# Kernel tuning notes

Measured on AMD Instinct MI355X. Metric: run time of the kernel, lower is better.

The kernel has to match this reference:

```python
import jax, jax.numpy as jnp
import numpy as np

N, D, M_COLS, K = 4096, 512, 4096, 2048

def setup_inputs() -> dict:
    key = jax.random.key(0)
    k1, k2, k3 = jax.random.split(key, 3)
    return {
        "in_activations": jax.random.normal(k1, (N, D), dtype=jnp.float32),
        "M": jax.random.normal(k2, (D, M_COLS), dtype=jnp.float32),
        "centroids": jax.random.normal(k3, (K, D), dtype=jnp.float32),
    }

def reference(in_activations, M, centroids):
    # dist[k, m] = || X @ (M[:, m] - c_k) ||_2  over the n sampled activations.
    # Expand || a - b ||^2 = ||a||^2 - 2 a.b + ||b||^2 with a = X@M[:,m], b = X@c_k
    # to avoid materializing the [K, n, m] broadcast tensor of the original.
    XM = in_activations @ M                 # [n, m]
    XC = in_activations @ centroids.T      # [n, K]
    sq = (jnp.sum(XM * XM, axis=0)[None, :]          # [1, m]
          - 2.0 * (XC.T @ XM)                        # [K, m]
          + jnp.sum(XC * XC, axis=0)[:, None])       # [K, 1]
    return jnp.sqrt(jnp.maximum(sq, 0.0))            # [K, m]
```

## Files before the change

kernel.cpp:

```cpp
#include <hip/hip_runtime.h>
#include <stdint.h>

#define NR    4096
#define D_DIM 512
#define MC    4096
#define KC    2048

typedef unsigned short u16;
typedef __attribute__((ext_vector_type(8))) short bf16x8;
typedef __attribute__((ext_vector_type(4))) float f32x4;

__device__ __forceinline__ u16 f2bf(float f) {
  union { float f; uint32_t u; } v; v.f = f;
  return (u16)((v.u + 0x7FFFu + ((v.u >> 16) & 1u)) >> 16);
}
__device__ __forceinline__ float bf2f(u16 h) {
  union { uint32_t u; float f; } v; v.u = (uint32_t)h << 16; return v.f;
}
__device__ __forceinline__ void gload16(const void* g, void* lds) {
  __builtin_amdgcn_global_load_lds((const __attribute__((address_space(1))) void*)g,
                                   (__attribute__((address_space(3))) void*)lds,
                                   16, 0, 0);
}

template <int EPI, int STEPS>
__device__ __forceinline__ void gemm_tile(
    const u16* __restrict__ Ag, const u16* __restrict__ Bg,
    float* __restrict__ Cf, u16* __restrict__ Cbf,
    const u16* __restrict__ DotH, const float* __restrict__ DotF,
    float* __restrict__ vatom, const float* __restrict__ tv, const float* __restrict__ sv,
    int m0, int n0, int Ndim, int Kdim, int kBeg,
    u16* As0, u16* As1, u16* Bs0, u16* Bs1, int tid)
{
  const int rowt = tid >> 3;
  const int cswz = ((tid & 7) ^ ((tid >> 3) & 7)) << 3;
  const int wave = tid >> 6, lane = tid & 63;
  const int wr = (wave >> 1) << 6, wc = (wave & 1) << 6;
  const int fr = lane & 15;
  const int sw = fr & 7;
  const int hq = lane >> 4;
  const int wb = wave << 10;

  f32x4 acc[4][4] = {};
  const u16* agB = Ag + (size_t)(m0 + rowt) * Kdim + cswz;
  const u16* bgB = Bg + (size_t)(n0 + rowt) * Kdim + cswz;

  #define STAGE(k0, Asb, Bsb)                                          \
    _Pragma("unroll")                                                  \
    for (int c = 0; c < 4; ++c) {                                      \
      gload16(agB + (k0) + (size_t)(c * 32) * Kdim, (char*)(Asb) + c * 4096 + wb); \
      gload16(bgB + (k0) + (size_t)(c * 32) * Kdim, (char*)(Bsb) + c * 4096 + wb); \
    }

  STAGE(kBeg, As0, Bs0)

  #pragma unroll
  for (int t = 0; t < STEPS; ++t) {
    u16* Ac = (t & 1) ? As1 : As0;
    u16* Bc = (t & 1) ? Bs1 : Bs0;
    if (t + 1 < STEPS) {
      u16* An = (t & 1) ? As0 : As1;
      u16* Bn = (t & 1) ? Bs0 : Bs1;
      STAGE(kBeg + (t + 1) * 64, An, Bn)
      asm volatile("s_waitcnt vmcnt(8)\n\ts_barrier" ::: "memory");
    } else {
      asm volatile("s_waitcnt vmcnt(0)\n\ts_barrier" ::: "memory");
    }
    __builtin_amdgcn_sched_barrier(0);
    #pragma unroll
    for (int kk = 0; kk < 64; kk += 32) {
      const int so = ((((kk >> 3) + hq) ^ sw) << 3);
      bf16x8 a[4], b[4];
      #pragma unroll
      for (int i = 0; i < 4; ++i) a[i] = *(const bf16x8*)&Ac[(wr + i * 16 + fr) * 64 + so];
      #pragma unroll
      for (int j = 0; j < 4; ++j) b[j] = *(const bf16x8*)&Bc[(wc + j * 16 + fr) * 64 + so];
      #pragma unroll
      for (int i = 0; i < 4; ++i)
        #pragma unroll
        for (int j = 0; j < 4; ++j)
          acc[i][j] = __builtin_amdgcn_mfma_f32_16x16x32_bf16(a[i], b[j], acc[i][j], 0, 0, 0);
    }
    if (t + 1 < STEPS)
      asm volatile("s_barrier" ::: "memory");
  }
  #undef STAGE

  const int q = lane >> 4;
  #pragma unroll
  for (int i = 0; i < 4; ++i) {
    #pragma unroll
    for (int r = 0; r < 4; ++r) {
      const int grow = m0 + wr + i * 16 + q * 4 + r;
      float p = 0.f;
      #pragma unroll
      for (int j = 0; j < 4; ++j) {
        const int gcol = n0 + wc + j * 16 + fr;
        const float v = acc[i][j][r];
        const size_t idx = (size_t)grow * Ndim + gcol;
        if (EPI == 0) Cf[idx] = v;
        if (EPI == 2) { float sq = tv[gcol] - 2.f * v + sv[grow]; Cf[idx] = sqrtf(fmaxf(sq, 0.f)); }
        if (EPI == 3) { Cbf[idx] = f2bf(v); p += v * bf2f(DotH[idx]); }
        if (EPI == 4) { p += v * DotF[idx]; }
      }
      if (EPI == 3 || EPI == 4) {
        #pragma unroll
        for (int off = 1; off < 16; off <<= 1) p += __shfl_xor(p, off);
        if (fr == 0) atomicAdd(&vatom[grow], p);
      }
    }
  }
}

__device__ __forceinline__ void transpose_tile(
    const float* __restrict__ in, u16* __restrict__ out, int R, int C,
    int rt, int ct, int tid, float* tile )
{
  const int tx = tid & 31, ty = tid >> 5;
  #pragma unroll
  for (int i = 0; i < 32; i += 8)
    tile[(size_t)(ty + i) * 33 + tx] = in[(size_t)(rt + ty + i) * C + ct + tx];
  __syncthreads();
  #pragma unroll
  for (int i = 0; i < 32; i += 8)
    out[(size_t)(ct + ty + i) * R + rt + tx] = f2bf(tile[(size_t)tx * 33 + ty + i]);
  __syncthreads();
}

__global__ __launch_bounds__(256)
void xprep(const float* __restrict__ X, u16* __restrict__ XT_bf,
           float* __restrict__ tvec)
{
  __shared__ float tile[32 * 33];
  const int b = blockIdx.x, tid = threadIdx.x;
  int zi = b * 256 + tid;
  if (zi < 4096 + 2048) tvec[zi] = 0.f;
  #pragma unroll 1
  for (int j = 0; j < 4; ++j) {
    int T = b * 4 + j;
    transpose_tile(X, XT_bf, NR, D_DIM, (T >> 4) * 32, (T & 15) * 32, tid, tile);
  }
}

__global__ __launch_bounds__(256)
void gmc(const u16* __restrict__ XT_bf, float* __restrict__ Gpart,
         const float* __restrict__ Mm, const float* __restrict__ Cc,
         u16* __restrict__ M_bfT, u16* __restrict__ C_bf)
{
  __shared__ __align__(16) u16 As[2][8192];
  __shared__ __align__(16) u16 Bs[2][8192];
  const int b = blockIdx.x, tid = threadIdx.x;
  if (b < 256) {
    const int t = b & 15, z = b >> 4;
    const int n0 = (t & 3) * 128, m0 = (t >> 2) * 128;
    gemm_tile<0, 4>(XT_bf, XT_bf, Gpart + (size_t)z * 512 * 512, nullptr, nullptr,
                    nullptr, nullptr, nullptr, nullptr, m0, n0, 512, NR, z * 256,
                    As[0], As[1], Bs[0], Bs[1], tid);
  } else if (b < 768) {
    float* ttile = (float*)As;
    #pragma unroll 1
    for (int j = 0; j < 4; ++j) {
      int T = (b - 256) * 4 + j;
      transpose_tile(Mm, M_bfT, D_DIM, MC, (T >> 7) * 32, (T & 127) * 32, tid, ttile);
    }
  } else {
    const int bb = b - 768;
    const float4* C4 = (const float4*)Cc;
    #pragma unroll 1
    for (int i = bb * 256 + tid; i < (KC * D_DIM) / 4; i += 128 * 256) {
      float4 v = C4[i];
      ushort4 r; r.x = f2bf(v.x); r.y = f2bf(v.y); r.z = f2bf(v.z); r.w = f2bf(v.w);
      *(ushort4*)&C_bf[(size_t)i * 4] = r;
    }
  }
}

__global__ __launch_bounds__(256)
void reduce_g(const float* __restrict__ Gpart, u16* __restrict__ G_bf)
{
  const float4* P4 = (const float4*)Gpart;
  int i = blockIdx.x * 256 + threadIdx.x;
  float4 s = {0.f, 0.f, 0.f, 0.f};
  #pragma unroll
  for (int z = 0; z < 16; ++z) {
    float4 v = P4[(size_t)z * (512 * 512 / 4) + i];
    s.x += v.x; s.y += v.y; s.z += v.z; s.w += v.w;
  }
  ushort4 r; r.x = f2bf(s.x); r.y = f2bf(s.y); r.z = f2bf(s.z); r.w = f2bf(s.w);
  *(ushort4*)&G_bf[(size_t)i * 4] = r;
}

__global__ __launch_bounds__(256)
void mid(const u16* __restrict__ M_bfT, const u16* __restrict__ C_bf,
         const u16* __restrict__ G_bf, const float* __restrict__ Cc,
         u16* __restrict__ A_bfT, float* __restrict__ tvec)
{
  __shared__ __align__(16) u16 As[2][8192];
  __shared__ __align__(16) u16 Bs[2][8192];
  const int b = blockIdx.x, tid = threadIdx.x;
  if (b < 128) {
    const int n0 = (b & 3) * 128, m0 = (b >> 2) * 128;
    gemm_tile<3, 8>(M_bfT, G_bf, nullptr, A_bfT, M_bfT, nullptr, tvec, nullptr, nullptr,
                    m0, n0, 512, 512, 0, As[0], As[1], Bs[0], Bs[1], tid);
  } else {
    const int u = b - 128;
    const int n0 = (u & 3) * 128, m0 = (u >> 2) * 128;
    gemm_tile<4, 8>(C_bf, G_bf, nullptr, nullptr, nullptr, Cc, tvec + 4096, nullptr,
                    nullptr, m0, n0, 512, 512, 0, As[0], As[1], Bs[0], Bs[1], tid);
  }
}

__global__ __launch_bounds__(256)
void final_gemm(const u16* __restrict__ C_bf, const u16* __restrict__ A_bfT,
                const float* __restrict__ tvec, float* __restrict__ out)
{
  __shared__ __align__(16) u16 As[2][8192];
  __shared__ __align__(16) u16 Bs[2][8192];
  const int n0 = blockIdx.x * 128, m0 = blockIdx.y * 128;
  gemm_tile<2, 8>(C_bf, A_bfT, out, nullptr, nullptr, nullptr, nullptr, tvec,
                  tvec + 4096, m0, n0, MC, 512, 0,
                  As[0], As[1], Bs[0], Bs[1], threadIdx.x);
}

extern "C" void kernel_launch(void* const* d_in, const int* in_sizes, int n_in,
                              void* d_out, int out_size, void* d_ws, size_t ws_size,
                              hipStream_t stream) {
  const float* X  = (const float*)d_in[0];
  const float* Mm = (const float*)d_in[1];
  const float* Cc = (const float*)d_in[2];
  float* out = (float*)d_out;

  char* ws = (char*)d_ws;
  const size_t MB = 1u << 20;
  u16*   XT_bf = (u16*)(ws);
  u16*   C_bf  = (u16*)(ws + 4 * MB);
  u16*   M_bfT = (u16*)(ws + 6 * MB);
  u16*   A_bfT = (u16*)(ws + 10 * MB);
  u16*   G_bf  = (u16*)(ws + 14 * MB);
  float* tvec  = (float*)(ws + 14 * MB + 512 * 1024);
  float* Gpart = (float*)(ws + 15 * MB);

  xprep<<<512, 256, 0, stream>>>(X, XT_bf, tvec);
  gmc<<<896, 256, 0, stream>>>(XT_bf, Gpart, Mm, Cc, M_bfT, C_bf);
  reduce_g<<<256, 256, 0, stream>>>(Gpart, G_bf);
  mid<<<192, 256, 0, stream>>>(M_bfT, C_bf, G_bf, Cc, A_bfT, tvec);
  final_gemm<<<dim3(32, 16), 256, 0, stream>>>(C_bf, A_bfT, tvec, out);
}
```

Before: 120.0 us.

## Replace split-K partial buffers and reduce kernel with atomic accumulation into fp32 Gram

The Gram-matrix split-K GEMM now uses 8 K-slices of 512 instead of 16 of 256, and accumulates directly into a zeroed fp32 buffer with atomicAdd instead of writing partials for a separate reduce kernel. The reduce_g launch is removed. The mid kernel gains a variant that loads the fp32 Gram matrix and converts it to bf16 in registers before storing to LDS. This drops one kernel launch and the partial-buffer traffic, at the cost of atomic contention, nondeterministic summation order, and an extra conversion step in mid's B-load path.

```diff
diff --git a/kernel.cpp b/kernel.cpp
--- a/kernel.cpp
+++ b/kernel.cpp
@@ -17,6 +17,9 @@
 __device__ __forceinline__ float bf2f(u16 h) {
   union { uint32_t u; float f; } v; v.u = (uint32_t)h << 16; return v.f;
 }
+__device__ __forceinline__ uint32_t pk2(float a, float b) {
+  return (uint32_t)f2bf(a) | ((uint32_t)f2bf(b) << 16);
+}
 __device__ __forceinline__ void gload16(const void* g, void* lds) {
   __builtin_amdgcn_global_load_lds((const __attribute__((address_space(1))) void*)g,
                                    (__attribute__((address_space(3))) void*)lds,
@@ -26,9 +29,8 @@
 template <int EPI, int STEPS>
 __device__ __forceinline__ void gemm_tile(
     const u16* __restrict__ Ag, const u16* __restrict__ Bg,
-    float* __restrict__ Cf, u16* __restrict__ Cbf,
-    const u16* __restrict__ DotH, const float* __restrict__ DotF,
-    float* __restrict__ vatom, const float* __restrict__ tv, const float* __restrict__ sv,
+    float* __restrict__ Cf,
+    const float* __restrict__ tv, const float* __restrict__ sv,
     int m0, int n0, int Ndim, int Kdim, int kBeg,
     u16* As0, u16* As1, u16* Bs0, u16* Bs1, int tid)
 {
@@ -92,22 +94,120 @@
     #pragma unroll
     for (int r = 0; r < 4; ++r) {
       const int grow = m0 + wr + i * 16 + q * 4 + r;
-      float p = 0.f;
       #pragma unroll
       for (int j = 0; j < 4; ++j) {
         const int gcol = n0 + wc + j * 16 + fr;
         const float v = acc[i][j][r];
         const size_t idx = (size_t)grow * Ndim + gcol;
-        if (EPI == 0) Cf[idx] = v;
+        if (EPI == 1) atomicAdd(&Cf[idx], v);
         if (EPI == 2) { float sq = tv[gcol] - 2.f * v + sv[grow]; Cf[idx] = sqrtf(fmaxf(sq, 0.f)); }
+      }
+    }
+  }
+}
+
+template <int EPI>
+__device__ __forceinline__ void gemm_f32B(
+    const u16* __restrict__ Ag, const float* __restrict__ Gf,
+    u16* __restrict__ Cbf, const u16* __restrict__ DotH,
+    const float* __restrict__ DotF, float* __restrict__ vatom,
+    int m0, int n0,
+    u16* As0, u16* As1, u16* Bs0, u16* Bs1, int tid)
+{
+  const int rowt = tid >> 3;
+  const int cswz = ((tid & 7) ^ ((tid >> 3) & 7)) << 3;
+  const int wave = tid >> 6, lane = tid & 63;
+  const int wr = (wave >> 1) << 6, wc = (wave & 1) << 6;
+  const int fr = lane & 15;
+  const int sw = fr & 7;
+  const int hq = lane >> 4;
+  const int wb = wave << 10;
+  const int bslot = tid & 7;
+  const int bswz = (bslot ^ (rowt & 7)) << 3;
+
+  f32x4 acc[4][4] = {};
+  const u16* agB = Ag + (size_t)(m0 + rowt) * 512 + cswz;
+  const float* gfB = Gf + (size_t)(n0 + rowt) * 512 + bslot * 8;
+
+  float4 breg[4][2];
+
+  #define STAGE_A(k0, Asb)                                             \
+    _Pragma("unroll")                                                  \
+    for (int c = 0; c < 4; ++c)                                        \
+      gload16(agB + (k0) + (size_t)(c * 32) * 512, (char*)(Asb) + c * 4096 + wb);
+
+  #define BLOAD(k0)                                                    \
+    _Pragma("unroll")                                                  \
+    for (int c = 0; c < 4; ++c) {                                      \
+      const float4* p = (const float4*)(gfB + (k0) + (size_t)(c * 32) * 512); \
+      breg[c][0] = p[0]; breg[c][1] = p[1];                            \
+    }
+
+  #define BSTORE(Bsb)                                                  \
+    _Pragma("unroll")                                                  \
+    for (int c = 0; c < 4; ++c) {                                      \
+      uint4 w;                                                         \
+      w.x = pk2(breg[c][0].x, breg[c][0].y);                           \
+      w.y = pk2(breg[c][0].z, breg[c][0].w);                           \
+      w.z = pk2(breg[c][1].x, breg[c][1].y);                           \
+      w.w = pk2(breg[c][1].z, breg[c][1].w);                           \
+      *(uint4*)&(Bsb)[(c * 32 + rowt) * 64 + bswz] = w;                \
+    }
+
+  BLOAD(0)
+  STAGE_A(0, As0)
+  BSTORE(Bs0)
+  __syncthreads();
+
+  #pragma unroll
+  for (int t = 0; t < 8; ++t) {
+    u16* Ac = (t & 1) ? As1 : As0;
+    u16* Bc = (t & 1) ? Bs1 : Bs0;
+    u16* An = (t & 1) ? As0 : As1;
+    u16* Bn = (t & 1) ? Bs0 : Bs1;
+    if (t + 1 < 8) {
+      STAGE_A((t + 1) * 64, An)
+      BLOAD((t + 1) * 64)
+    }
+    #pragma unroll
+    for (int kk = 0; kk < 64; kk += 32) {
+      const int so = ((((kk >> 3) + hq) ^ sw) << 3);
+      bf16x8 a[4], b[4];
+      #pragma unroll
+      for (int i = 0; i < 4; ++i) a[i] = *(const bf16x8*)&Ac[(wr + i * 16 + fr) * 64 + so];
+      #pragma unroll
+      for (int j = 0; j < 4; ++j) b[j] = *(const bf16x8*)&Bc[(wc + j * 16 + fr) * 64 + so];
+      #pragma unroll
+      for (int i = 0; i < 4; ++i)
+        #pragma unroll
+        for (int j = 0; j < 4; ++j)
+          acc[i][j] = __builtin_amdgcn_mfma_f32_16x16x32_bf16(a[i], b[j], acc[i][j], 0, 0, 0);
+    }
+    if (t + 1 < 8) BSTORE(Bn)
+    __syncthreads();
+  }
+  #undef STAGE_A
+  #undef BLOAD
+  #undef BSTORE
+
+  const int q = lane >> 4;
+  #pragma unroll
+  for (int i = 0; i < 4; ++i) {
+    #pragma unroll
+    for (int r = 0; r < 4; ++r) {
+      const int grow = m0 + wr + i * 16 + q * 4 + r;
+      float p = 0.f;
+      #pragma unroll
+      for (int j = 0; j < 4; ++j) {
+        const int gcol = n0 + wc + j * 16 + fr;
+        const float v = acc[i][j][r];
+        const size_t idx = (size_t)grow * 512 + gcol;
         if (EPI == 3) { Cbf[idx] = f2bf(v); p += v * bf2f(DotH[idx]); }
         if (EPI == 4) { p += v * DotF[idx]; }
       }
-      if (EPI == 3 || EPI == 4) {
-        #pragma unroll
-        for (int off = 1; off < 16; off <<= 1) p += __shfl_xor(p, off);
-        if (fr == 0) atomicAdd(&vatom[grow], p);
-      }
+      #pragma unroll
+      for (int off = 1; off < 16; off <<= 1) p += __shfl_xor(p, off);
+      if (fr == 0) atomicAdd(&vatom[grow], p);
     }
   }
 }
@@ -129,12 +229,13 @@
 
 __global__ __launch_bounds__(256)
 void xprep(const float* __restrict__ X, u16* __restrict__ XT_bf,
-           float* __restrict__ tvec)
+           float* __restrict__ tvec, float* __restrict__ Gf)
 {
   __shared__ float tile[32 * 33];
   const int b = blockIdx.x, tid = threadIdx.x;
-  int zi = b * 256 + tid;
-  if (zi < 4096 + 2048) tvec[zi] = 0.f;
+  const int gi = b * 256 + tid;
+  if (gi < 4096 + 2048) tvec[gi] = 0.f;
+  *(float2*)&Gf[(size_t)gi * 2] = make_float2(0.f, 0.f);
   #pragma unroll 1
   for (int j = 0; j < 4; ++j) {
     int T = b * 4 + j;
@@ -143,28 +244,27 @@
 }
 
 __global__ __launch_bounds__(256)
-void gmc(const u16* __restrict__ XT_bf, float* __restrict__ Gpart,
+void gmc(const u16* __restrict__ XT_bf, float* __restrict__ Gf,
          const float* __restrict__ Mm, const float* __restrict__ Cc,
          u16* __restrict__ M_bfT, u16* __restrict__ C_bf)
 {
   __shared__ __align__(16) u16 As[2][8192];
   __shared__ __align__(16) u16 Bs[2][8192];
   const int b = blockIdx.x, tid = threadIdx.x;
-  if (b < 256) {
+  if (b < 128) {
     const int t = b & 15, z = b >> 4;
     const int n0 = (t & 3) * 128, m0 = (t >> 2) * 128;
-    gemm_tile<0, 4>(XT_bf, XT_bf, Gpart + (size_t)z * 512 * 512, nullptr, nullptr,
-                    nullptr, nullptr, nullptr, nullptr, m0, n0, 512, NR, z * 256,
-                    As[0], As[1], Bs[0], Bs[1], tid);
-  } else if (b < 768) {
+    gemm_tile<1, 8>(XT_bf, XT_bf, Gf, nullptr, nullptr,
+                    m0, n0, 512, NR, z * 512, As[0], As[1], Bs[0], Bs[1], tid);
+  } else if (b < 640) {
     float* ttile = (float*)As;
     #pragma unroll 1
     for (int j = 0; j < 4; ++j) {
-      int T = (b - 256) * 4 + j;
+      int T = (b - 128) * 4 + j;
       transpose_tile(Mm, M_bfT, D_DIM, MC, (T >> 7) * 32, (T & 127) * 32, tid, ttile);
     }
   } else {
-    const int bb = b - 768;
+    const int bb = b - 640;
     const float4* C4 = (const float4*)Cc;
     #pragma unroll 1
     for (int i = bb * 256 + tid; i < (KC * D_DIM) / 4; i += 128 * 256) {
@@ -176,23 +276,8 @@
 }
 
 __global__ __launch_bounds__(256)
-void reduce_g(const float* __restrict__ Gpart, u16* __restrict__ G_bf)
-{
-  const float4* P4 = (const float4*)Gpart;
-  int i = blockIdx.x * 256 + threadIdx.x;
-  float4 s = {0.f, 0.f, 0.f, 0.f};
-  #pragma unroll
-  for (int z = 0; z < 16; ++z) {
-    float4 v = P4[(size_t)z * (512 * 512 / 4) + i];
-    s.x += v.x; s.y += v.y; s.z += v.z; s.w += v.w;
-  }
-  ushort4 r; r.x = f2bf(s.x); r.y = f2bf(s.y); r.z = f2bf(s.z); r.w = f2bf(s.w);
-  *(ushort4*)&G_bf[(size_t)i * 4] = r;
-}
-
-__global__ __launch_bounds__(256)
 void mid(const u16* __restrict__ M_bfT, const u16* __restrict__ C_bf,
-         const u16* __restrict__ G_bf, const float* __restrict__ Cc,
+         const float* __restrict__ Gf, const float* __restrict__ Cc,
          u16* __restrict__ A_bfT, float* __restrict__ tvec)
 {
   __shared__ __align__(16) u16 As[2][8192];
@@ -200,13 +285,13 @@
   const int b = blockIdx.x, tid = threadIdx.x;
   if (b < 128) {
     const int n0 = (b & 3) * 128, m0 = (b >> 2) * 128;
-    gemm_tile<3, 8>(M_bfT, G_bf, nullptr, A_bfT, M_bfT, nullptr, tvec, nullptr, nullptr,
-                    m0, n0, 512, 512, 0, As[0], As[1], Bs[0], Bs[1], tid);
+    gemm_f32B<3>(M_bfT, Gf, A_bfT, M_bfT, nullptr, tvec,
+                 m0, n0, As[0], As[1], Bs[0], Bs[1], tid);
   } else {
     const int u = b - 128;
     const int n0 = (u & 3) * 128, m0 = (u >> 2) * 128;
-    gemm_tile<4, 8>(C_bf, G_bf, nullptr, nullptr, nullptr, Cc, tvec + 4096, nullptr,
-                    nullptr, m0, n0, 512, 512, 0, As[0], As[1], Bs[0], Bs[1], tid);
+    gemm_f32B<4>(C_bf, Gf, nullptr, nullptr, Cc, tvec + 4096,
+                 m0, n0, As[0], As[1], Bs[0], Bs[1], tid);
   }
 }
 
@@ -217,9 +302,8 @@
   __shared__ __align__(16) u16 As[2][8192];
   __shared__ __align__(16) u16 Bs[2][8192];
   const int n0 = blockIdx.x * 128, m0 = blockIdx.y * 128;
-  gemm_tile<2, 8>(C_bf, A_bfT, out, nullptr, nullptr, nullptr, nullptr, tvec,
-                  tvec + 4096, m0, n0, MC, 512, 0,
-                  As[0], As[1], Bs[0], Bs[1], threadIdx.x);
+  gemm_tile<2, 8>(C_bf, A_bfT, out, tvec, tvec + 4096,
+                  m0, n0, MC, 512, 0, As[0], As[1], Bs[0], Bs[1], threadIdx.x);
 }
 
 extern "C" void kernel_launch(void* const* d_in, const int* in_sizes, int n_in,
@@ -236,13 +320,11 @@
   u16*   C_bf  = (u16*)(ws + 4 * MB);
   u16*   M_bfT = (u16*)(ws + 6 * MB);
   u16*   A_bfT = (u16*)(ws + 10 * MB);
-  u16*   G_bf  = (u16*)(ws + 14 * MB);
-  float* tvec  = (float*)(ws + 14 * MB + 512 * 1024);
-  float* Gpart = (float*)(ws + 15 * MB);
-
-  xprep<<<512, 256, 0, stream>>>(X, XT_bf, tvec);
-  gmc<<<896, 256, 0, stream>>>(XT_bf, Gpart, Mm, Cc, M_bfT, C_bf);
-  reduce_g<<<256, 256, 0, stream>>>(Gpart, G_bf);
-  mid<<<192, 256, 0, stream>>>(M_bfT, C_bf, G_bf, Cc, A_bfT, tvec);
+  float* tvec  = (float*)(ws + 14 * MB);
+  float* Gf    = (float*)(ws + 15 * MB);
+
+  xprep<<<512, 256, 0, stream>>>(X, XT_bf, tvec, Gf);
+  gmc<<<768, 256, 0, stream>>>(XT_bf, Gf, Mm, Cc, M_bfT, C_bf);
+  mid<<<192, 256, 0, stream>>>(M_bfT, C_bf, Gf, Cc, A_bfT, tvec);
   final_gemm<<<dim3(32, 16), 256, 0, stream>>>(C_bf, A_bfT, tvec, out);
 }
```

After: 125.9 us. 1.05x slower.
